# Optimization experiments

Hardware: AMD Instinct MI355X
Metric: run time of the kernel (lower is better)

The kernel has to match this reference:

```python
import jax, jax.numpy as jnp
import numpy as np

T = 0.07  # NT-Xent temperature (init arg t)
VOL = (64, 128, 128)
C = 32
N = 2048


def setup_inputs() -> dict:
    key = jax.random.key(0)
    k0, k1, k2, k3 = jax.random.split(key, 4)
    e0 = jax.random.normal(k0, (1, C) + VOL, dtype=jnp.float32)
    e1 = jax.random.normal(k1, (1, C) + VOL, dtype=jnp.float32)
    # embeddings are assumed L2-normalized over channels
    e0 = e0 / jnp.linalg.norm(e0, axis=1, keepdims=True)
    e1 = e1 / jnp.linalg.norm(e1, axis=1, keepdims=True)
    dims = jnp.array(VOL, dtype=jnp.int32)
    loc0 = jax.random.randint(k2, (1, N, 3), 0, dims).astype(jnp.float32)
    loc1 = jax.random.randint(k3, (1, N, 3), 0, dims).astype(jnp.float32)
    return {"emb_0": e0, "emb_1": e1, "locations_0": loc0, "locations_1": loc1}


def reference(emb_0, emb_1, locations_0, locations_1):
    b, c = emb_0.shape[0], emb_0.shape[1]
    vol = emb_0.shape[2:]
    v = int(np.prod(vol))
    n = locations_0.shape[1]
    # (b, c, *vol) -> (b, v, c)
    e0 = emb_0.reshape(b, c, v).transpose(0, 2, 1)
    e1 = emb_1.reshape(b, c, v).transpose(0, 2, 1)
    # flatten integer coordinates to linear indices (row-major strides)
    kernel = jnp.array([np.prod(vol[i + 1:]) for i in range(len(vol))], dtype=jnp.float32)
    ind_0 = (jnp.floor(locations_0) @ kernel).astype(jnp.int32)[0]  # (n,)
    ind_1 = (jnp.floor(locations_1) @ kernel).astype(jnp.int32)[0]  # (n,)
    g0 = jnp.take(e0, ind_0, axis=1)  # (b, n, c)
    g1 = jnp.take(e1, ind_1, axis=1)  # (b, n, c)
    emb = jnp.concatenate([g0, g1], axis=1)  # (b, 2n, c)
    sim = jnp.einsum('bnc,bmc->bnm', emb, emb)  # (b, 2n, 2n)
    exp = jnp.exp(sim / T)
    # sum over non-diagonal entries of each row
    sum_e = exp.sum(axis=2) - jnp.diagonal(exp, axis1=1, axis2=2)  # (b, 2n)
    idx = jnp.arange(n)
    e_uv = exp[:, idx, idx + n]  # (b, n) positive-pair terms
    loss = -jnp.sum(jnp.log(e_uv / sum_e[:, :n]) + jnp.log(e_uv / sum_e[:, n:]))
    return loss / (2 * n)
```

## Files before the change

### kernel.cpp

```cpp
#include <hip/hip_runtime.h>

#define NPTS   2048
#define NROWS  (2 * NPTS)
#define CCH    32
#define VOL_V  (64 * 128 * 128)
#define INV_T  (1.0f / 0.07f)
#define NCHUNK 16

typedef __attribute__((ext_vector_type(8))) short bf16x8;
typedef __attribute__((ext_vector_type(4))) float f32x4;

__global__ __launch_bounds__(256) void gather_k(
    const float* __restrict__ e0, const float* __restrict__ e1,
    const float* __restrict__ loc0, const float* __restrict__ loc1,
    unsigned short* __restrict__ Eb, float* __restrict__ out)
{
    int idx = blockIdx.x * 256 + threadIdx.x;
    if (idx == 0) out[0] = 0.0f;
    if (idx >= NROWS * CCH) return;
    int r = idx >> 5;
    int c = idx & 31;
    const float* loc = (r < NPTS) ? (loc0 + 3 * r) : (loc1 + 3 * (r - NPTS));
    const float* e   = (r < NPTS) ? e0 : e1;
    int ind = (int)loc[0] * 16384 + (int)loc[1] * 128 + (int)loc[2];
    float v = e[(size_t)c * VOL_V + ind];
    unsigned u = __builtin_bit_cast(unsigned, v);
    u += 0x7fff + ((u >> 16) & 1);
    Eb[idx] = (unsigned short)(u >> 16);
}

__global__ __launch_bounds__(256) void rowsum_k(
    const unsigned short* __restrict__ Eb, float* __restrict__ partial)
{
    int lane    = threadIdx.x & 63;
    int wave_id = blockIdx.x * 4 + (threadIdx.x >> 6);
    int rstripe = wave_id & (NROWS / 32 - 1);
    int chunk   = wave_id >> 7;
    int r0      = rstripe * 32;

    int lrow = lane & 15;
    int lgrp = lane >> 4;
    int koff = lgrp * 8;

    bf16x8 a0 = *(const bf16x8*)(Eb + (size_t)(r0      + lrow) * CCH + koff);
    bf16x8 a1 = *(const bf16x8*)(Eb + (size_t)(r0 + 16 + lrow) * CCH + koff);

    float racc0[4] = {0.f, 0.f, 0.f, 0.f};
    float racc1[4] = {0.f, 0.f, 0.f, 0.f};
    int rg_base0 = r0      + lgrp * 4;
    int rg_base1 = r0 + 16 + lgrp * 4;

    const f32x4 zero = {0.f, 0.f, 0.f, 0.f};

    #pragma unroll 4
    for (int t = 0; t < 256 / 16 / NCHUNK * 16; ++t) {
        int j0 = (chunk * 16 + t) * 16;
        bf16x8 b = *(const bf16x8*)(Eb + (size_t)(j0 + lrow) * CCH + koff);
        f32x4 c0 = __builtin_amdgcn_mfma_f32_16x16x32_bf16(a0, b, zero, 0, 0, 0);
        f32x4 c1 = __builtin_amdgcn_mfma_f32_16x16x32_bf16(a1, b, zero, 0, 0, 0);
        int jg = j0 + lrow;
        #pragma unroll
        for (int q = 0; q < 4; ++q) {
            float ex0 = __expf(c0[q] * INV_T);
            float ex1 = __expf(c1[q] * INV_T);
            racc0[q] += (jg == rg_base0 + q) ? 0.0f : ex0;
            racc1[q] += (jg == rg_base1 + q) ? 0.0f : ex1;
        }
    }

    #pragma unroll
    for (int q = 0; q < 4; ++q) {
        #pragma unroll
        for (int m = 1; m < 16; m <<= 1) {
            racc0[q] += __shfl_xor(racc0[q], m);
            racc1[q] += __shfl_xor(racc1[q], m);
        }
    }
    if (lrow == 0) {
        #pragma unroll
        for (int q = 0; q < 4; ++q) {
            partial[(size_t)chunk * NROWS + rg_base0 + q] = racc0[q];
            partial[(size_t)chunk * NROWS + rg_base1 + q] = racc1[q];
        }
    }
}

__global__ __launch_bounds__(256) void finalize_k(
    const unsigned short* __restrict__ Eb, const float* __restrict__ partial,
    float* __restrict__ out)
{
    __shared__ float red[256];
    int r = blockIdx.x * 256 + threadIdx.x;

    float rs = 0.0f;
    #pragma unroll
    for (int ch = 0; ch < NCHUNK; ++ch)
        rs += partial[(size_t)ch * NROWS + r];

    int p = (r < NPTS) ? (r + NPTS) : (r - NPTS);
    float s = 0.0f;
    #pragma unroll
    for (int c = 0; c < CCH; ++c) {
        float a = __builtin_bit_cast(float, (unsigned)Eb[(size_t)r * CCH + c] << 16);
        float b = __builtin_bit_cast(float, (unsigned)Eb[(size_t)p * CCH + c] << 16);
        s = fmaf(a, b, s);
    }

    float contrib = s * INV_T - __logf(rs);

    red[threadIdx.x] = contrib;
    __syncthreads();
    #pragma unroll
    for (int off = 128; off > 0; off >>= 1) {
        if (threadIdx.x < off) red[threadIdx.x] += red[threadIdx.x + off];
        __syncthreads();
    }
    if (threadIdx.x == 0)
        atomicAdd(out, -red[0] / (2.0f * NPTS));
}

extern "C" void kernel_launch(void* const* d_in, const int* in_sizes, int n_in,
                              void* d_out, int out_size, void* d_ws, size_t ws_size,
                              hipStream_t stream)
{
    const float* e0 = (const float*)d_in[0];
    const float* e1 = (const float*)d_in[1];
    const float* l0 = (const float*)d_in[2];
    const float* l1 = (const float*)d_in[3];
    float* out = (float*)d_out;

    unsigned short* Eb = (unsigned short*)d_ws;
    float* partial = (float*)((char*)d_ws + (size_t)NROWS * CCH * 2);

    gather_k<<<(NROWS * CCH + 255) / 256, 256, 0, stream>>>(e0, e1, l0, l1, Eb, out);

    int nwaves = (NROWS / 32) * NCHUNK;
    rowsum_k<<<nwaves / 4, 256, 0, stream>>>(Eb, partial);

    finalize_k<<<NROWS / 256, 256, 0, stream>>>(Eb, partial, out);
}
```

Measured before the change: 21.39 us.

## Fuse finalize into rowsum via last-block atomic counter and halve chunk count

Removes the separate finalize kernel launch. The last rowsum block, detected with an atomic counter and threadfence, reduces the partial row sums, computes positive-pair dot products with vectorized bf16 loads, and writes the loss directly. NCHUNK drops from 16 to 8, so each wave covers twice as many column tiles and there are fewer partials to reduce. The trade-off is a serialized single-block tail and lower parallelism in the main kernel.

```diff
diff --git a/kernel.cpp b/kernel.cpp
--- a/kernel.cpp
+++ b/kernel.cpp
@@ -5,7 +5,7 @@
 #define CCH    32
 #define VOL_V  (64 * 128 * 128)
 #define INV_T  (1.0f / 0.07f)
-#define NCHUNK 16
+#define NCHUNK 8
 
 typedef __attribute__((ext_vector_type(8))) short bf16x8;
 typedef __attribute__((ext_vector_type(4))) float f32x4;
@@ -13,10 +13,10 @@
 __global__ __launch_bounds__(256) void gather_k(
     const float* __restrict__ e0, const float* __restrict__ e1,
     const float* __restrict__ loc0, const float* __restrict__ loc1,
-    unsigned short* __restrict__ Eb, float* __restrict__ out)
+    unsigned short* __restrict__ Eb, int* __restrict__ cnt)
 {
     int idx = blockIdx.x * 256 + threadIdx.x;
-    if (idx == 0) out[0] = 0.0f;
+    if (idx == 0) cnt[0] = 0;
     if (idx >= NROWS * CCH) return;
     int r = idx >> 5;
     int c = idx & 31;
@@ -30,7 +30,8 @@
 }
 
 __global__ __launch_bounds__(256) void rowsum_k(
-    const unsigned short* __restrict__ Eb, float* __restrict__ partial)
+    const unsigned short* __restrict__ Eb, float* __restrict__ partial,
+    int* __restrict__ cnt, float* __restrict__ out)
 {
     int lane    = threadIdx.x & 63;
     int wave_id = blockIdx.x * 4 + (threadIdx.x >> 6);
@@ -53,8 +54,8 @@
     const f32x4 zero = {0.f, 0.f, 0.f, 0.f};
 
     #pragma unroll 4
-    for (int t = 0; t < 256 / 16 / NCHUNK * 16; ++t) {
-        int j0 = (chunk * 16 + t) * 16;
+    for (int t = 0; t < 256 / NCHUNK; ++t) {
+        int j0 = (chunk * (256 / NCHUNK) + t) * 16;
         bf16x8 b = *(const bf16x8*)(Eb + (size_t)(j0 + lrow) * CCH + koff);
         f32x4 c0 = __builtin_amdgcn_mfma_f32_16x16x32_bf16(a0, b, zero, 0, 0, 0);
         f32x4 c1 = __builtin_amdgcn_mfma_f32_16x16x32_bf16(a1, b, zero, 0, 0, 0);
@@ -83,32 +84,44 @@
             partial[(size_t)chunk * NROWS + rg_base1 + q] = racc1[q];
         }
     }
-}
 
-__global__ __launch_bounds__(256) void finalize_k(
-    const unsigned short* __restrict__ Eb, const float* __restrict__ partial,
-    float* __restrict__ out)
-{
-    __shared__ float red[256];
-    int r = blockIdx.x * 256 + threadIdx.x;
+    __threadfence();
+    __syncthreads();
+    __shared__ int is_last;
+    if (threadIdx.x == 0)
+        is_last = (atomicAdd(cnt, 1) == (int)gridDim.x - 1);
+    __syncthreads();
+    if (!is_last) return;
+    __threadfence();
 
-    float rs = 0.0f;
-    #pragma unroll
-    for (int ch = 0; ch < NCHUNK; ++ch)
-        rs += partial[(size_t)ch * NROWS + r];
+    float lsum = 0.0f;
+    #pragma unroll 2
+    for (int rr = 0; rr < NROWS / 256; ++rr) {
+        int r = rr * 256 + threadIdx.x;
+        float rs = 0.0f;
+        #pragma unroll
+        for (int ch = 0; ch < NCHUNK; ++ch)
+            rs += partial[(size_t)ch * NROWS + r];
 
-    int p = (r < NPTS) ? (r + NPTS) : (r - NPTS);
-    float s = 0.0f;
-    #pragma unroll
-    for (int c = 0; c < CCH; ++c) {
-        float a = __builtin_bit_cast(float, (unsigned)Eb[(size_t)r * CCH + c] << 16);
-        float b = __builtin_bit_cast(float, (unsigned)Eb[(size_t)p * CCH + c] << 16);
-        s = fmaf(a, b, s);
+        int p = r ^ NPTS;
+        const bf16x8* er = (const bf16x8*)(Eb + (size_t)r * CCH);
+        const bf16x8* ep = (const bf16x8*)(Eb + (size_t)p * CCH);
+        float s = 0.0f;
+        #pragma unroll
+        for (int i = 0; i < 4; ++i) {
+            bf16x8 va = er[i], vb = ep[i];
+            #pragma unroll
+            for (int k = 0; k < 8; ++k) {
+                float fa = __builtin_bit_cast(float, (unsigned)(unsigned short)va[k] << 16);
+                float fb = __builtin_bit_cast(float, (unsigned)(unsigned short)vb[k] << 16);
+                s = fmaf(fa, fb, s);
+            }
+        }
+        lsum += s * INV_T - __logf(rs);
     }
 
-    float contrib = s * INV_T - __logf(rs);
-
-    red[threadIdx.x] = contrib;
+    __shared__ float red[256];
+    red[threadIdx.x] = lsum;
     __syncthreads();
     #pragma unroll
     for (int off = 128; off > 0; off >>= 1) {
@@ -116,7 +129,7 @@
         __syncthreads();
     }
     if (threadIdx.x == 0)
-        atomicAdd(out, -red[0] / (2.0f * NPTS));
+        out[0] = -red[0] / (2.0f * NPTS);
 }
 
 extern "C" void kernel_launch(void* const* d_in, const int* in_sizes, int n_in,
@@ -131,11 +144,11 @@
 
     unsigned short* Eb = (unsigned short*)d_ws;
     float* partial = (float*)((char*)d_ws + (size_t)NROWS * CCH * 2);
+    int* cnt = (int*)((char*)d_ws + (size_t)NROWS * CCH * 2
+                                  + (size_t)NCHUNK * NROWS * 4);
 
-    gather_k<<<(NROWS * CCH + 255) / 256, 256, 0, stream>>>(e0, e1, l0, l1, Eb, out);
+    gather_k<<<(NROWS * CCH + 255) / 256, 256, 0, stream>>>(e0, e1, l0, l1, Eb, cnt);
 
-    int nwaves = (NROWS / 32) * NCHUNK;
-    rowsum_k<<<nwaves / 4, 256, 0, stream>>>(Eb, partial);
-
-    finalize_k<<<NROWS / 256, 256, 0, stream>>>(Eb, partial, out);
+    int nblocks = (NROWS / 32) * NCHUNK / 4;
+    rowsum_k<<<nblocks, 256, 0, stream>>>(Eb, partial, cnt, out);
 }
```

Result: slower. 52.40 us (+145.0%).

## Fuse finalize into rowsum kernel with in-block reduction and pair extraction

Applied to the files above, without the earlier changes.

Removes the separate finalize kernel by having each block own 16 rows across all columns (4 waves splitting the column range), reducing row sums through LDS and picking the positive-pair similarity directly from the MFMA output. Each block then computes its loss contribution and atomically adds it to the output. This drops one kernel launch and the partial-sum buffer round trip. In exchange, each wave now issues one MFMA per B tile instead of two, so B reuse is halved, and the extra pair-select adds ALU work per element.

```diff
diff --git a/kernel.cpp b/kernel.cpp
--- a/kernel.cpp
+++ b/kernel.cpp
@@ -5,7 +5,6 @@
 #define CCH    32
 #define VOL_V  (64 * 128 * 128)
 #define INV_T  (1.0f / 0.07f)
-#define NCHUNK 16
 
 typedef __attribute__((ext_vector_type(8))) short bf16x8;
 typedef __attribute__((ext_vector_type(4))) float f32x4;
@@ -30,41 +29,34 @@
 }
 
 __global__ __launch_bounds__(256) void rowsum_k(
-    const unsigned short* __restrict__ Eb, float* __restrict__ partial)
+    const unsigned short* __restrict__ Eb, float* __restrict__ out)
 {
-    int lane    = threadIdx.x & 63;
-    int wave_id = blockIdx.x * 4 + (threadIdx.x >> 6);
-    int rstripe = wave_id & (NROWS / 32 - 1);
-    int chunk   = wave_id >> 7;
-    int r0      = rstripe * 32;
-
+    int lane = threadIdx.x & 63;
+    int w    = threadIdx.x >> 6;
+    int r0   = blockIdx.x * 16;
     int lrow = lane & 15;
     int lgrp = lane >> 4;
     int koff = lgrp * 8;
 
-    bf16x8 a0 = *(const bf16x8*)(Eb + (size_t)(r0      + lrow) * CCH + koff);
-    bf16x8 a1 = *(const bf16x8*)(Eb + (size_t)(r0 + 16 + lrow) * CCH + koff);
+    bf16x8 a = *(const bf16x8*)(Eb + (size_t)(r0 + lrow) * CCH + koff);
 
-    float racc0[4] = {0.f, 0.f, 0.f, 0.f};
-    float racc1[4] = {0.f, 0.f, 0.f, 0.f};
-    int rg_base0 = r0      + lgrp * 4;
-    int rg_base1 = r0 + 16 + lgrp * 4;
+    float racc[4]  = {0.f, 0.f, 0.f, 0.f};
+    float pairv[4] = {0.f, 0.f, 0.f, 0.f};
+    int rg = r0 + lgrp * 4;
 
     const f32x4 zero = {0.f, 0.f, 0.f, 0.f};
 
-    #pragma unroll 4
-    for (int t = 0; t < 256 / 16 / NCHUNK * 16; ++t) {
-        int j0 = (chunk * 16 + t) * 16;
+    #pragma unroll 8
+    for (int t = 0; t < 64; ++t) {
+        int j0 = (w * 64 + t) * 16;
         bf16x8 b = *(const bf16x8*)(Eb + (size_t)(j0 + lrow) * CCH + koff);
-        f32x4 c0 = __builtin_amdgcn_mfma_f32_16x16x32_bf16(a0, b, zero, 0, 0, 0);
-        f32x4 c1 = __builtin_amdgcn_mfma_f32_16x16x32_bf16(a1, b, zero, 0, 0, 0);
+        f32x4 c = __builtin_amdgcn_mfma_f32_16x16x32_bf16(a, b, zero, 0, 0, 0);
         int jg = j0 + lrow;
         #pragma unroll
         for (int q = 0; q < 4; ++q) {
-            float ex0 = __expf(c0[q] * INV_T);
-            float ex1 = __expf(c1[q] * INV_T);
-            racc0[q] += (jg == rg_base0 + q) ? 0.0f : ex0;
-            racc1[q] += (jg == rg_base1 + q) ? 0.0f : ex1;
+            float ex = __expf(c[q] * INV_T);
+            racc[q] += (jg == rg + q) ? 0.0f : ex;
+            pairv[q] = (jg == ((rg + q) ^ NPTS)) ? c[q] : pairv[q];
         }
     }
 
@@ -72,51 +64,33 @@
     for (int q = 0; q < 4; ++q) {
         #pragma unroll
         for (int m = 1; m < 16; m <<= 1) {
-            racc0[q] += __shfl_xor(racc0[q], m);
-            racc1[q] += __shfl_xor(racc1[q], m);
+            racc[q]  += __shfl_xor(racc[q], m);
+            pairv[q] += __shfl_xor(pairv[q], m);
         }
     }
+
+    __shared__ float lds_rs[4][16];
+    __shared__ float lds_ps[4][16];
     if (lrow == 0) {
         #pragma unroll
         for (int q = 0; q < 4; ++q) {
-            partial[(size_t)chunk * NROWS + rg_base0 + q] = racc0[q];
-            partial[(size_t)chunk * NROWS + rg_base1 + q] = racc1[q];
+            lds_rs[w][lgrp * 4 + q] = racc[q];
+            lds_ps[w][lgrp * 4 + q] = pairv[q];
         }
     }
-}
+    __syncthreads();
 
-__global__ __launch_bounds__(256) void finalize_k(
-    const unsigned short* __restrict__ Eb, const float* __restrict__ partial,
-    float* __restrict__ out)
-{
-    __shared__ float red[256];
-    int r = blockIdx.x * 256 + threadIdx.x;
-
-    float rs = 0.0f;
-    #pragma unroll
-    for (int ch = 0; ch < NCHUNK; ++ch)
-        rs += partial[(size_t)ch * NROWS + r];
-
-    int p = (r < NPTS) ? (r + NPTS) : (r - NPTS);
-    float s = 0.0f;
-    #pragma unroll
-    for (int c = 0; c < CCH; ++c) {
-        float a = __builtin_bit_cast(float, (unsigned)Eb[(size_t)r * CCH + c] << 16);
-        float b = __builtin_bit_cast(float, (unsigned)Eb[(size_t)p * CCH + c] << 16);
-        s = fmaf(a, b, s);
+    if (threadIdx.x < 16) {
+        int row = threadIdx.x;
+        float rs = lds_rs[0][row] + lds_rs[1][row] + lds_rs[2][row] + lds_rs[3][row];
+        float ps = lds_ps[0][row] + lds_ps[1][row] + lds_ps[2][row] + lds_ps[3][row];
+        float contrib = ps * INV_T - __logf(rs);
+        #pragma unroll
+        for (int m = 1; m < 16; m <<= 1)
+            contrib += __shfl_xor(contrib, m);
+        if (row == 0)
+            atomicAdd(out, -contrib / (2.0f * NPTS));
     }
-
-    float contrib = s * INV_T - __logf(rs);
-
-    red[threadIdx.x] = contrib;
-    __syncthreads();
-    #pragma unroll
-    for (int off = 128; off > 0; off >>= 1) {
-        if (threadIdx.x < off) red[threadIdx.x] += red[threadIdx.x + off];
-        __syncthreads();
-    }
-    if (threadIdx.x == 0)
-        atomicAdd(out, -red[0] / (2.0f * NPTS));
 }
 
 extern "C" void kernel_launch(void* const* d_in, const int* in_sizes, int n_in,
@@ -130,12 +104,8 @@
     float* out = (float*)d_out;
 
     unsigned short* Eb = (unsigned short*)d_ws;
-    float* partial = (float*)((char*)d_ws + (size_t)NROWS * CCH * 2);
 
-    gather_k<<<(NROWS * CCH + 255) / 256, 256, 0, stream>>>(e0, e1, l0, l1, Eb, out);
+    gather_k<<<(NROWS * CCH) / 256, 256, 0, stream>>>(e0, e1, l0, l1, Eb, out);
 
-    int nwaves = (NROWS / 32) * NCHUNK;
-    rowsum_k<<<nwaves / 4, 256, 0, stream>>>(Eb, partial);
-
-    finalize_k<<<NROWS / 256, 256, 0, stream>>>(Eb, partial, out);
+    rowsum_k<<<NROWS / 16, 256, 0, stream>>>(Eb, out);
 }
```

Measured after the change: 34.92 us. +63.3%, slower.
